# Performance work log

Hardware: AMD Instinct MI355X
Metric: run time of the kernel (lower is better)

The kernel has to match this reference:

```python
import jax, jax.numpy as jnp
import numpy as np

B, S, H, F, E, TOPK = 2, 2048, 1024, 512, 8, 2


def setup_inputs() -> dict:
    key = jax.random.key(0)
    k1, k2, k3, k4, k5 = jax.random.split(key, 5)
    s_h = 1.0 / np.sqrt(H)
    s_f = 1.0 / np.sqrt(F)
    return {
        "x": jax.random.normal(k1, (B, S, H), dtype=jnp.float32),
        "Wr": jax.random.normal(k2, (H, E), dtype=jnp.float32) * s_h,   # router
        "Wg": jax.random.normal(k3, (E, H, F), dtype=jnp.float32) * s_h,  # gate proj
        "Wu": jax.random.normal(k4, (E, H, F), dtype=jnp.float32) * s_h,  # up proj
        "Wd": jax.random.normal(k5, (E, F, H), dtype=jnp.float32) * s_f,  # down proj
        "topk": TOPK,
    }


def reference(x, Wr, Wg, Wu, Wd, topk):
    Bq, Sq, Hq = x.shape
    Eq = Wr.shape[1]
    xf = x.reshape(-1, Hq)                      # [T, H]
    logits = xf @ Wr                            # [T, E]
    probs = jax.nn.softmax(logits, axis=-1)
    w, idx = jax.lax.top_k(probs, topk)         # [T, topk]
    w = w / jnp.sum(w, axis=-1, keepdims=True)  # normalize top-k probs (Qwen3-style)
    # combine coefficients per (token, expert): scatter top-k weights
    coeff = jnp.sum(jax.nn.one_hot(idx, Eq, dtype=w.dtype) * w[..., None], axis=1)  # [T, E]
    # dense dispatch/combine (math-equivalent to per-expert gather + scatter-add)
    gate = jnp.einsum('th,ehf->tef', xf, Wg)    # [T, E, F]
    up = jnp.einsum('th,ehf->tef', xf, Wu)
    act = jax.nn.silu(gate) * up                # SwiGLU expert
    # apply combine weight before down-proj (linearity) to avoid a [T,E,H] temp
    out = jnp.einsum('tef,efh->th', act * coeff[:, :, None], Wd)
    return out.reshape(Bq, Sq, Hq)
```

## Files before the change

### kernel.cpp

```cpp
#include <hip/hip_runtime.h>
#include <hip/hip_bf16.h>

#define T_TOK    4096
#define H_DIM    1024
#define F_DIM    512
#define N_EXP    8
#define N_ASSIGN 8192
#define BM 128
#define BN 128
#define BK 64
#define MAX_TILES 80
#define GRID_MT   71
#define TRU      3072

typedef __bf16 bf16x8 __attribute__((ext_vector_type(8)));
typedef float  f32x4  __attribute__((ext_vector_type(4)));

#define MFMA16(a, b, c) __builtin_amdgcn_mfma_f32_16x16x32_bf16((a), (b), (c), 0, 0, 0)

__device__ __forceinline__ void gl_lds16(const __bf16* g, __bf16* l) {
    __builtin_amdgcn_global_load_lds(
        (const __attribute__((address_space(1))) unsigned int*)g,
        (__attribute__((address_space(3))) unsigned int*)l,
        16, 0, 0);
}

__global__ __launch_bounds__(256) void transpose_kernel(
    const float* __restrict__ Wg, const float* __restrict__ Wu, const float* __restrict__ Wd,
    __bf16* __restrict__ Wcat, __bf16* __restrict__ Wdt)
{
    __shared__ float tile[64][65];
    int b = blockIdx.x, tid = threadIdx.x;
    const float* src; int C, z, c0, r0;
    if (b < 2048) {
        z = b >> 7; int rem = b & 127;
        c0 = (rem & 7) * 64; r0 = (rem >> 3) * 64;
        src = (z < 8) ? Wg + (size_t)z * H_DIM * F_DIM
                      : Wu + (size_t)(z - 8) * H_DIM * F_DIM;
        C = F_DIM;
    } else {
        int v = b - 2048; z = 16 + (v >> 7); int rem = v & 127;
        c0 = (rem & 15) * 64; r0 = (rem >> 4) * 64;
        src = Wd + (size_t)(z - 16) * F_DIM * H_DIM;
        C = H_DIM;
    }
    int fr = tid >> 4, f4 = tid & 15;
#pragma unroll
    for (int p = 0; p < 4; ++p) {
        int row = p * 16 + fr;
        float4 v = *(const float4*)(src + (size_t)(r0 + row) * C + c0 + f4 * 4);
        tile[row][f4 * 4 + 0] = v.x; tile[row][f4 * 4 + 1] = v.y;
        tile[row][f4 * 4 + 2] = v.z; tile[row][f4 * 4 + 3] = v.w;
    }
    __syncthreads();
    int j = tid & 7, cl = tid >> 3;
#pragma unroll
    for (int p = 0; p < 2; ++p) {
        int c = cl + p * 32;
        bf16x8 v;
#pragma unroll
        for (int i = 0; i < 8; ++i) v[i] = (__bf16)tile[8 * j + i][c];
        if (z < 16) {
            int e = (z < 8) ? z : z - 8;
            int sel = (z < 8) ? 0 : 16;
            int f = c0 + c;
            int pp = ((f >> 4) << 5) + (f & 15) + sel;
            *(bf16x8*)&Wcat[(size_t)e * 2 * F_DIM * H_DIM + (size_t)pp * H_DIM + r0 + 8 * j] = v;
        } else {
            *(bf16x8*)&Wdt[(size_t)(z - 16) * H_DIM * F_DIM + (size_t)(c0 + c) * F_DIM + r0 + 8 * j] = v;
        }
    }
}

__global__ __launch_bounds__(256) void routing_kernel(
    const float* __restrict__ x, const float* __restrict__ Wr,
    __bf16* __restrict__ xb, int* __restrict__ top_e, float* __restrict__ top_w)
{
    __shared__ float WrS[N_EXP * H_DIM];
    int tid = threadIdx.x;
    for (int i = tid; i < N_EXP * H_DIM; i += 256) {
        int h = i >> 3, e = i & 7;
        WrS[e * H_DIM + h] = Wr[i];
    }
    __syncthreads();

    int wave = tid >> 6, lane = tid & 63;
    int t = blockIdx.x * 4 + wave;
    const float* xrow = x + (size_t)t * H_DIM;
    __bf16* xbrow = xb + (size_t)t * H_DIM;

    float part[N_EXP];
#pragma unroll
    for (int e = 0; e < N_EXP; ++e) part[e] = 0.f;
#pragma unroll 4
    for (int s = 0; s < 16; ++s) {
        int h = s * 64 + lane;
        float xs = xrow[h];
        xbrow[h] = (__bf16)xs;
#pragma unroll
        for (int e = 0; e < N_EXP; ++e) part[e] += xs * WrS[e * H_DIM + h];
    }
#pragma unroll
    for (int m = 1; m < 64; m <<= 1) {
#pragma unroll
        for (int e = 0; e < N_EXP; ++e) part[e] += __shfl_xor(part[e], m, 64);
    }
    if (lane == 0) {
        float v1 = -1e30f, v2 = -1e30f;
        int i1 = 0, i2 = 0;
#pragma unroll
        for (int e = 0; e < N_EXP; ++e) {
            float p = part[e];
            if (p > v1)      { v2 = v1; i2 = i1; v1 = p; i1 = e; }
            else if (p > v2) { v2 = p;  i2 = e; }
        }
        float w1 = 1.f / (1.f + __expf(v2 - v1));
        top_e[t * 2]     = i1;  top_e[t * 2 + 1] = i2;
        top_w[t * 2]     = w1;  top_w[t * 2 + 1] = 1.f - w1;
    }
}

__global__ __launch_bounds__(256) void sort_kernel(
    const int* __restrict__ top_e, const float* __restrict__ top_w,
    int* __restrict__ perm, float* __restrict__ wts, int* __restrict__ tokslot,
    int* __restrict__ tile_e, int* __restrict__ tile_m0, int* __restrict__ tile_cnt,
    int* __restrict__ n_tiles)
{
    __shared__ int hist[N_EXP][256];
    __shared__ int ebase[N_EXP];
    int tid = threadIdx.x, myexp = blockIdx.x;
    int c[N_EXP];
#pragma unroll
    for (int e = 0; e < N_EXP; ++e) c[e] = 0;
#pragma unroll 4
    for (int i = 0; i < 32; ++i) {
        int ee = top_e[tid * 32 + i];
#pragma unroll
        for (int e = 0; e < N_EXP; ++e) c[e] += (ee == e);
    }
#pragma unroll
    for (int e = 0; e < N_EXP; ++e) hist[e][tid] = c[e];
    __syncthreads();
    for (int s = 1; s < 256; s <<= 1) {
        int v[N_EXP];
#pragma unroll
        for (int e = 0; e < N_EXP; ++e) v[e] = (tid >= s) ? hist[e][tid - s] : 0;
        __syncthreads();
#pragma unroll
        for (int e = 0; e < N_EXP; ++e) hist[e][tid] += v[e];
        __syncthreads();
    }
    if (tid == 0) {
        int o = 0, nt = 0;
        for (int e = 0; e < N_EXP; ++e) {
            ebase[e] = o;
            int ne = hist[e][255];
            if (myexp == 0) {
                for (int m0 = 0; m0 < ne; m0 += BM) {
                    tile_e[nt]   = e;
                    tile_m0[nt]  = o + m0;
                    tile_cnt[nt] = (ne - m0 < BM) ? (ne - m0) : BM;
                    ++nt;
                }
            }
            o += ne;
        }
        if (myexp == 0) *n_tiles = nt;
    }
    __syncthreads();
    int base = ebase[myexp] + hist[myexp][tid] - c[myexp];
#pragma unroll 4
    for (int i = 0; i < 32; ++i) {
        int a = tid * 32 + i;
        if (top_e[a] == myexp) {
            perm[base]   = a >> 1;
            wts[base]    = top_w[a];
            tokslot[a]   = base;
            ++base;
        }
    }
}

__global__ __launch_bounds__(256, 3) void gateup_kernel(
    const __bf16* __restrict__ xb, const __bf16* __restrict__ Wcat,
    const int* __restrict__ perm, const float* __restrict__ wts,
    const int* __restrict__ tile_e, const int* __restrict__ tile_m0, const int* __restrict__ tile_cnt,
    const int* __restrict__ n_tiles, __bf16* __restrict__ act)
{
    int mt = blockIdx.x >> 3;
    if (mt >= *n_tiles) return;
    int e = tile_e[mt], m0 = tile_m0[mt], mcnt = tile_cnt[mt];
    int n0 = (blockIdx.x & 7) * BN;
    __shared__ __align__(16) __bf16 As[BM * BK];
    __shared__ __align__(16) __bf16 Bs[BN * BK];
    __shared__ int   rowtok[BM];
    __shared__ float roww[BM];
    int tid = threadIdx.x;
    if (tid < BM) {
        int slot = m0 + ((tid < mcnt) ? tid : 0);
        rowtok[tid] = perm[slot];
        roww[tid]   = wts[slot];
    }
    __syncthreads();
    int wave = tid >> 6, lane = tid & 63;
    int srow   = wave * 8 + (lane >> 3);
    int schunk = (((lane & 7) ^ ((lane >> 3) & 7))) * 8;
    const __bf16* We = Wcat + (size_t)e * (2 * F_DIM) * H_DIM;
    const __bf16* aptr[4];
    const __bf16* bptr[4];
#pragma unroll
    for (int j = 0; j < 4; ++j) {
        int r = j * 32 + srow;
        aptr[j] = xb + (size_t)rowtok[r] * H_DIM + schunk;
        bptr[j] = We + (size_t)(n0 + r) * H_DIM + schunk;
    }
    __bf16* aLds = As + wave * 512;
    __bf16* bLds = Bs + wave * 512;
    int wm = wave & 1, wn = wave >> 1;
    int quad = lane >> 4, l16 = lane & 15;
    f32x4 acc[4][4];
#pragma unroll
    for (int a = 0; a < 4; ++a)
#pragma unroll
        for (int b = 0; b < 4; ++b) acc[a][b] = (f32x4){0.f, 0.f, 0.f, 0.f};
    for (int k0 = 0; k0 < H_DIM; k0 += BK) {
#pragma unroll
        for (int j = 0; j < 4; ++j) {
            gl_lds16(aptr[j] + k0, aLds + j * 2048);
            gl_lds16(bptr[j] + k0, bLds + j * 2048);
        }
        __syncthreads();
#pragma unroll
        for (int s = 0; s < 2; ++s) {
            int sw = (((quad + s * 4) ^ (l16 & 7))) * 8;
            bf16x8 af[4], bf[4];
#pragma unroll
            for (int im = 0; im < 4; ++im)
                af[im] = *(const bf16x8*)&As[(wm * 64 + im * 16 + l16) * 64 + sw];
#pragma unroll
            for (int in = 0; in < 4; ++in)
                bf[in] = *(const bf16x8*)&Bs[(wn * 64 + in * 16 + l16) * 64 + sw];
#pragma unroll
            for (int im = 0; im < 4; ++im)
#pragma unroll
                for (int in = 0; in < 4; ++in)
                    acc[im][in] = MFMA16(af[im], bf[in], acc[im][in]);
        }
        __syncthreads();
    }
    int fbase = (n0 >> 1) + wn * 32;
#pragma unroll
    for (int im = 0; im < 4; ++im) {
#pragma unroll
        for (int ip = 0; ip < 2; ++ip) {
            f32x4 g = acc[im][ip * 2], u = acc[im][ip * 2 + 1];
            int fcol = fbase + ip * 16 + l16;
#pragma unroll
            for (int r = 0; r < 4; ++r) {
                int rl = wm * 64 + im * 16 + quad * 4 + r;
                if (rl < mcnt) {
                    float gv = g[r], uv = u[r];
                    float sg = gv / (1.f + __expf(-gv));
                    act[(size_t)(m0 + rl) * F_DIM + fcol] = (__bf16)(sg * uv * roww[rl]);
                }
            }
        }
    }
}

__global__ __launch_bounds__(256, 3) void down_kernel(
    const __bf16* __restrict__ act, const __bf16* __restrict__ Wdt,
    const int* __restrict__ tile_e, const int* __restrict__ tile_m0, const int* __restrict__ tile_cnt,
    const int* __restrict__ n_tiles, __bf16* __restrict__ P)
{
    int mt = blockIdx.x >> 3;
    if (mt >= *n_tiles) return;
    int e = tile_e[mt], m0 = tile_m0[mt], mcnt = tile_cnt[mt];
    int n0 = (blockIdx.x & 7) * BN;
    __shared__ __align__(16) __bf16 As[BM * BK];
    __shared__ __align__(16) __bf16 Bs[BN * BK];
    int tid = threadIdx.x;
    int wave = tid >> 6, lane = tid & 63;
    int srow   = wave * 8 + (lane >> 3);
    int schunk = (((lane & 7) ^ ((lane >> 3) & 7))) * 8;
    const __bf16* Wd_e = Wdt + (size_t)e * H_DIM * F_DIM;
    const __bf16* aptr[4];
    const __bf16* bptr[4];
#pragma unroll
    for (int j = 0; j < 4; ++j) {
        int r = j * 32 + srow;
        int ar = m0 + ((r < mcnt) ? r : 0);
        aptr[j] = act  + (size_t)ar * F_DIM + schunk;
        bptr[j] = Wd_e + (size_t)(n0 + r) * F_DIM + schunk;
    }
    __bf16* aLds = As + wave * 512;
    __bf16* bLds = Bs + wave * 512;
    int wm = wave & 1, wn = wave >> 1;
    int quad = lane >> 4, l16 = lane & 15;
    f32x4 acc[4][4];
#pragma unroll
    for (int a = 0; a < 4; ++a)
#pragma unroll
        for (int b = 0; b < 4; ++b) acc[a][b] = (f32x4){0.f, 0.f, 0.f, 0.f};
    for (int k0 = 0; k0 < F_DIM; k0 += BK) {
#pragma unroll
        for (int j = 0; j < 4; ++j) {
            gl_lds16(aptr[j] + k0, aLds + j * 2048);
            gl_lds16(bptr[j] + k0, bLds + j * 2048);
        }
        __syncthreads();
#pragma unroll
        for (int s = 0; s < 2; ++s) {
            int sw = (((quad + s * 4) ^ (l16 & 7))) * 8;
            bf16x8 af[4], bf[4];
#pragma unroll
            for (int im = 0; im < 4; ++im)
                af[im] = *(const bf16x8*)&As[(wm * 64 + im * 16 + l16) * 64 + sw];
#pragma unroll
            for (int in = 0; in < 4; ++in)
                bf[in] = *(const bf16x8*)&Bs[(wn * 64 + in * 16 + l16) * 64 + sw];
#pragma unroll
            for (int im = 0; im < 4; ++im)
#pragma unroll
                for (int in = 0; in < 4; ++in)
                    acc[im][in] = MFMA16(af[im], bf[in], acc[im][in]);
        }
        __syncthreads();
    }
#pragma unroll
    for (int im = 0; im < 4; ++im) {
#pragma unroll
        for (int in = 0; in < 4; ++in) {
            int col = n0 + wn * 64 + in * 16 + l16;
#pragma unroll
            for (int r = 0; r < 4; ++r) {
                int rl = wm * 64 + im * 16 + quad * 4 + r;
                if (rl < mcnt)
                    P[(size_t)(m0 + rl) * H_DIM + col] = (__bf16)acc[im][in][r];
            }
        }
    }
}

__global__ __launch_bounds__(256) void combine_kernel(
    const __bf16* __restrict__ P, const int* __restrict__ tokslot,
    float* __restrict__ out)
{
    int wave = threadIdx.x >> 6, lane = threadIdx.x & 63;
    int t = blockIdx.x * 4 + wave;
    int s1 = tokslot[2 * t], s2 = tokslot[2 * t + 1];
    const bf16x8* p1 = (const bf16x8*)(P + (size_t)s1 * H_DIM);
    const bf16x8* p2 = (const bf16x8*)(P + (size_t)s2 * H_DIM);
    float* o = out + (size_t)t * H_DIM;
#pragma unroll
    for (int i = 0; i < 2; ++i) {
        int idx = i * 64 + lane;
        bf16x8 a = p1[idx], b = p2[idx];
        f32x4 lo, hi;
#pragma unroll
        for (int j = 0; j < 4; ++j) lo[j] = (float)a[j] + (float)b[j];
#pragma unroll
        for (int j = 0; j < 4; ++j) hi[j] = (float)a[4 + j] + (float)b[4 + j];
        *(f32x4*)(o + idx * 8)     = lo;
        *(f32x4*)(o + idx * 8 + 4) = hi;
    }
}

extern "C" void kernel_launch(void* const* d_in, const int* in_sizes, int n_in,
                              void* d_out, int out_size, void* d_ws, size_t ws_size,
                              hipStream_t stream)
{
    const float* x  = (const float*)d_in[0];
    const float* Wr = (const float*)d_in[1];
    const float* Wg = (const float*)d_in[2];
    const float* Wu = (const float*)d_in[3];
    const float* Wd = (const float*)d_in[4];
    float* out = (float*)d_out;

    char* ws = (char*)d_ws;
    size_t off = 0;
    auto carve = [&](size_t bytes) {
        char* p = ws + off;
        off = (off + bytes + 255) & ~(size_t)255;
        return p;
    };
    __bf16* xb   = (__bf16*)carve((size_t)T_TOK * H_DIM * 2);
    __bf16* Wcat = (__bf16*)carve((size_t)N_EXP * 2 * F_DIM * H_DIM * 2);
    __bf16* Wdt  = (__bf16*)carve((size_t)N_EXP * H_DIM * F_DIM * 2);
    __bf16* act  = (__bf16*)carve((size_t)N_ASSIGN * F_DIM * 2);
    __bf16* P    = (__bf16*)carve((size_t)N_ASSIGN * H_DIM * 2);
    int*   top_e = (int*)carve((size_t)T_TOK * 2 * sizeof(int));
    float* top_w = (float*)carve((size_t)T_TOK * 2 * sizeof(float));
    int*   perm  = (int*)carve((size_t)N_ASSIGN * sizeof(int));
    float* wts   = (float*)carve((size_t)N_ASSIGN * sizeof(float));
    int*  tokslot= (int*)carve((size_t)N_ASSIGN * sizeof(int));
    int*   tl_e  = (int*)carve(MAX_TILES * sizeof(int));
    int*   tl_m0 = (int*)carve(MAX_TILES * sizeof(int));
    int*   tl_cn = (int*)carve(MAX_TILES * sizeof(int));
    int*   n_til = (int*)carve(sizeof(int));

    transpose_kernel<<<TRU, 256, 0, stream>>>(Wg, Wu, Wd, Wcat, Wdt);
    routing_kernel<<<T_TOK / 4, 256, 0, stream>>>(x, Wr, xb, top_e, top_w);
    sort_kernel<<<N_EXP, 256, 0, stream>>>(
        top_e, top_w, perm, wts, tokslot, tl_e, tl_m0, tl_cn, n_til);
    gateup_kernel<<<GRID_MT * 8, 256, 0, stream>>>(
        xb, Wcat, perm, wts, tl_e, tl_m0, tl_cn, n_til, act);
    down_kernel<<<GRID_MT * 8, 256, 0, stream>>>(
        act, Wdt, tl_e, tl_m0, tl_cn, n_til, P);
    combine_kernel<<<T_TOK / 4, 256, 0, stream>>>(P, tokslot, out);
}
```

Measured before the change: 192.4 us.

## Double-buffer LDS tiles in expert GEMMs and coalesce routing/sort accesses

Both expert GEMM kernels (gate/up and down) now keep two LDS buffers per operand, so the next K-slice's global-to-LDS load is issued while the MFMAs consume the current slice. This is meant to hide global load latency inside each block, but it doubles shared memory per block, so the occupancy hint drops from 3 to 2 blocks. The sort kernel now uses a strided assignment index so adjacent threads read adjacent top_e entries, and the routing kernel XOR-swizzles the router weights in LDS to cut bank conflicts. The sort change reorders tokens within each expert group, which stays consistent because counting and scatter use the same mapping.

```diff
diff --git a/kernel.cpp b/kernel.cpp
--- a/kernel.cpp
+++ b/kernel.cpp
@@ -80,7 +80,7 @@
     int tid = threadIdx.x;
     for (int i = tid; i < N_EXP * H_DIM; i += 256) {
         int h = i >> 3, e = i & 7;
-        WrS[e * H_DIM + h] = Wr[i];
+        WrS[e * H_DIM + (h ^ (e << 2))] = Wr[i];
     }
     __syncthreads();
 
@@ -98,7 +98,7 @@
         float xs = xrow[h];
         xbrow[h] = (__bf16)xs;
 #pragma unroll
-        for (int e = 0; e < N_EXP; ++e) part[e] += xs * WrS[e * H_DIM + h];
+        for (int e = 0; e < N_EXP; ++e) part[e] += xs * WrS[e * H_DIM + (h ^ (e << 2))];
     }
 #pragma unroll
     for (int m = 1; m < 64; m <<= 1) {
@@ -134,7 +134,7 @@
     for (int e = 0; e < N_EXP; ++e) c[e] = 0;
 #pragma unroll 4
     for (int i = 0; i < 32; ++i) {
-        int ee = top_e[tid * 32 + i];
+        int ee = top_e[i * 256 + tid];
 #pragma unroll
         for (int e = 0; e < N_EXP; ++e) c[e] += (ee == e);
     }
@@ -171,7 +171,7 @@
     int base = ebase[myexp] + hist[myexp][tid] - c[myexp];
 #pragma unroll 4
     for (int i = 0; i < 32; ++i) {
-        int a = tid * 32 + i;
+        int a = i * 256 + tid;
         if (top_e[a] == myexp) {
             perm[base]   = a >> 1;
             wts[base]    = top_w[a];
@@ -181,7 +181,7 @@
     }
 }
 
-__global__ __launch_bounds__(256, 3) void gateup_kernel(
+__global__ __launch_bounds__(256, 2) void gateup_kernel(
     const __bf16* __restrict__ xb, const __bf16* __restrict__ Wcat,
     const int* __restrict__ perm, const float* __restrict__ wts,
     const int* __restrict__ tile_e, const int* __restrict__ tile_m0, const int* __restrict__ tile_cnt,
@@ -191,8 +191,8 @@
     if (mt >= *n_tiles) return;
     int e = tile_e[mt], m0 = tile_m0[mt], mcnt = tile_cnt[mt];
     int n0 = (blockIdx.x & 7) * BN;
-    __shared__ __align__(16) __bf16 As[BM * BK];
-    __shared__ __align__(16) __bf16 Bs[BN * BK];
+    __shared__ __align__(16) __bf16 As[2][BM * BK];
+    __shared__ __align__(16) __bf16 Bs[2][BN * BK];
     __shared__ int   rowtok[BM];
     __shared__ float roww[BM];
     int tid = threadIdx.x;
@@ -214,8 +214,7 @@
         aptr[j] = xb + (size_t)rowtok[r] * H_DIM + schunk;
         bptr[j] = We + (size_t)(n0 + r) * H_DIM + schunk;
     }
-    __bf16* aLds = As + wave * 512;
-    __bf16* bLds = Bs + wave * 512;
+    int ldsoff = wave * 512;
     int wm = wave & 1, wn = wave >> 1;
     int quad = lane >> 4, l16 = lane & 15;
     f32x4 acc[4][4];
@@ -223,23 +222,36 @@
     for (int a = 0; a < 4; ++a)
 #pragma unroll
         for (int b = 0; b < 4; ++b) acc[a][b] = (f32x4){0.f, 0.f, 0.f, 0.f};
-    for (int k0 = 0; k0 < H_DIM; k0 += BK) {
-#pragma unroll
-        for (int j = 0; j < 4; ++j) {
-            gl_lds16(aptr[j] + k0, aLds + j * 2048);
-            gl_lds16(bptr[j] + k0, bLds + j * 2048);
-        }
-        __syncthreads();
+
+#pragma unroll
+    for (int j = 0; j < 4; ++j) {
+        gl_lds16(aptr[j], &As[0][ldsoff + j * 2048]);
+        gl_lds16(bptr[j], &Bs[0][ldsoff + j * 2048]);
+    }
+    __syncthreads();
+
+    for (int ks = 0; ks < H_DIM / BK; ++ks) {
+        int cur = ks & 1;
+        if (ks + 1 < H_DIM / BK) {
+            int k1 = (ks + 1) * BK;
+#pragma unroll
+            for (int j = 0; j < 4; ++j) {
+                gl_lds16(aptr[j] + k1, &As[cur ^ 1][ldsoff + j * 2048]);
+                gl_lds16(bptr[j] + k1, &Bs[cur ^ 1][ldsoff + j * 2048]);
+            }
+        }
+        const __bf16* Asc = As[cur];
+        const __bf16* Bsc = Bs[cur];
 #pragma unroll
         for (int s = 0; s < 2; ++s) {
             int sw = (((quad + s * 4) ^ (l16 & 7))) * 8;
             bf16x8 af[4], bf[4];
 #pragma unroll
             for (int im = 0; im < 4; ++im)
-                af[im] = *(const bf16x8*)&As[(wm * 64 + im * 16 + l16) * 64 + sw];
+                af[im] = *(const bf16x8*)&Asc[(wm * 64 + im * 16 + l16) * 64 + sw];
 #pragma unroll
             for (int in = 0; in < 4; ++in)
-                bf[in] = *(const bf16x8*)&Bs[(wn * 64 + in * 16 + l16) * 64 + sw];
+                bf[in] = *(const bf16x8*)&Bsc[(wn * 64 + in * 16 + l16) * 64 + sw];
 #pragma unroll
             for (int im = 0; im < 4; ++im)
 #pragma unroll
@@ -268,7 +280,7 @@
     }
 }
 
-__global__ __launch_bounds__(256, 3) void down_kernel(
+__global__ __launch_bounds__(256, 2) void down_kernel(
     const __bf16* __restrict__ act, const __bf16* __restrict__ Wdt,
     const int* __restrict__ tile_e, const int* __restrict__ tile_m0, const int* __restrict__ tile_cnt,
     const int* __restrict__ n_tiles, __bf16* __restrict__ P)
@@ -277,8 +289,8 @@
     if (mt >= *n_tiles) return;
     int e = tile_e[mt], m0 = tile_m0[mt], mcnt = tile_cnt[mt];
     int n0 = (blockIdx.x & 7) * BN;
-    __shared__ __align__(16) __bf16 As[BM * BK];
-    __shared__ __align__(16) __bf16 Bs[BN * BK];
+    __shared__ __align__(16) __bf16 As[2][BM * BK];
+    __shared__ __align__(16) __bf16 Bs[2][BN * BK];
     int tid = threadIdx.x;
     int wave = tid >> 6, lane = tid & 63;
     int srow   = wave * 8 + (lane >> 3);
@@ -293,8 +305,7 @@
         aptr[j] = act  + (size_t)ar * F_DIM + schunk;
         bptr[j] = Wd_e + (size_t)(n0 + r) * F_DIM + schunk;
     }
-    __bf16* aLds = As + wave * 512;
-    __bf16* bLds = Bs + wave * 512;
+    int ldsoff = wave * 512;
     int wm = wave & 1, wn = wave >> 1;
     int quad = lane >> 4, l16 = lane & 15;
     f32x4 acc[4][4];
@@ -302,23 +313,36 @@
     for (int a = 0; a < 4; ++a)
 #pragma unroll
         for (int b = 0; b < 4; ++b) acc[a][b] = (f32x4){0.f, 0.f, 0.f, 0.f};
-    for (int k0 = 0; k0 < F_DIM; k0 += BK) {
-#pragma unroll
-        for (int j = 0; j < 4; ++j) {
-            gl_lds16(aptr[j] + k0, aLds + j * 2048);
-            gl_lds16(bptr[j] + k0, bLds + j * 2048);
-        }
-        __syncthreads();
+
+#pragma unroll
+    for (int j = 0; j < 4; ++j) {
+        gl_lds16(aptr[j], &As[0][ldsoff + j * 2048]);
+        gl_lds16(bptr[j], &Bs[0][ldsoff + j * 2048]);
+    }
+    __syncthreads();
+
+    for (int ks = 0; ks < F_DIM / BK; ++ks) {
+        int cur = ks & 1;
+        if (ks + 1 < F_DIM / BK) {
+            int k1 = (ks + 1) * BK;
+#pragma unroll
+            for (int j = 0; j < 4; ++j) {
+                gl_lds16(aptr[j] + k1, &As[cur ^ 1][ldsoff + j * 2048]);
+                gl_lds16(bptr[j] + k1, &Bs[cur ^ 1][ldsoff + j * 2048]);
+            }
+        }
+        const __bf16* Asc = As[cur];
+        const __bf16* Bsc = Bs[cur];
 #pragma unroll
         for (int s = 0; s < 2; ++s) {
             int sw = (((quad + s * 4) ^ (l16 & 7))) * 8;
             bf16x8 af[4], bf[4];
 #pragma unroll
             for (int im = 0; im < 4; ++im)
-                af[im] = *(const bf16x8*)&As[(wm * 64 + im * 16 + l16) * 64 + sw];
+                af[im] = *(const bf16x8*)&Asc[(wm * 64 + im * 16 + l16) * 64 + sw];
 #pragma unroll
             for (int in = 0; in < 4; ++in)
-                bf[in] = *(const bf16x8*)&Bs[(wn * 64 + in * 16 + l16) * 64 + sw];
+                bf[in] = *(const bf16x8*)&Bsc[(wn * 64 + in * 16 + l16) * 64 + sw];
 #pragma unroll
             for (int im = 0; im < 4; ++im)
 #pragma unroll
```

New measurement: 206.4 us. 1.07x slower.
